# Optimization experiments

Measured on AMD Instinct MI355X. Metric: run time of the kernel, lower is better.

The kernel has to match this reference:

```python
import jax, jax.numpy as jnp
import numpy as np

B, N, K, H, L = 2, 1024, 48, 128, 3
SCALE = 30.0


def _gelu(x):
    # torch.nn.GELU default is the exact erf formulation
    return jax.nn.gelu(x, approximate=False)


def _ln(x, g, b, eps=1e-5):
    mu = jnp.mean(x, axis=-1, keepdims=True)
    var = jnp.mean((x - mu) ** 2, axis=-1, keepdims=True)
    return g * (x - mu) * jax.lax.rsqrt(var + eps) + b


def _gather_nodes(nodes, idx):
    # nodes: [B,N,H], idx: [B,N,K] -> [B,N,K,H]
    b, n, k = idx.shape
    flat = idx.reshape(b, n * k)
    g = jnp.take_along_axis(nodes, flat[:, :, None], axis=1)
    return g.reshape(b, n, k, nodes.shape[-1])


def setup_inputs() -> dict:
    key = jax.random.key(0)
    ks = jax.random.split(key, 16)

    def w(k, shape, fan_in):
        return jax.random.normal(k, shape, jnp.float32) / np.sqrt(fan_in).astype(np.float32)

    kp = jax.random.split(ks[5], 9)
    inp = {
        "h_V": jax.random.normal(ks[0], (B, N, H), jnp.float32),
        "h_E": jax.random.normal(ks[1], (B, N, K, H), jnp.float32),
        "E_idx": jax.random.randint(ks[2], (B, N, K), 0, N),
        "mask_V": jnp.ones((B, N), jnp.float32),
        "mask_attend": jnp.ones((B, N, K), jnp.float32),
        # message MLP (node update): W1 [3H->H], W2, W3
        "W1": w(kp[0], (L, 3 * H, H), 3 * H), "b1": jnp.zeros((L, H), jnp.float32),
        "W2": w(kp[1], (L, H, H), H), "b2": jnp.zeros((L, H), jnp.float32),
        "W3": w(kp[2], (L, H, H), H), "b3": jnp.zeros((L, H), jnp.float32),
        # message MLP (edge update): W11 [3H->H], W12, W13
        "W11": w(kp[3], (L, 3 * H, H), 3 * H), "b11": jnp.zeros((L, H), jnp.float32),
        "W12": w(kp[4], (L, H, H), H), "b12": jnp.zeros((L, H), jnp.float32),
        "W13": w(kp[5], (L, H, H), H), "b13": jnp.zeros((L, H), jnp.float32),
        # position-wise FFN: H -> 4H -> H
        "Win": w(kp[6], (L, H, 4 * H), H), "bin_": jnp.zeros((L, 4 * H), jnp.float32),
        "Wout": w(kp[7], (L, 4 * H, H), 4 * H), "bout": jnp.zeros((L, H), jnp.float32),
        # LayerNorms
        "g1": jnp.ones((L, H), jnp.float32), "be1": jnp.zeros((L, H), jnp.float32),
        "g2": jnp.ones((L, H), jnp.float32), "be2": jnp.zeros((L, H), jnp.float32),
        "g3": jnp.ones((L, H), jnp.float32), "be3": jnp.zeros((L, H), jnp.float32),
    }
    return inp


def reference(h_V, h_E, E_idx, mask_V, mask_attend,
              W1, b1, W2, b2, W3, b3,
              W11, b11, W12, b12, W13, b13,
              Win, bin_, Wout, bout,
              g1, be1, g2, be2, g3, be3):
    # Stack of L EncLayers (eval mode, dropout = identity).
    for l in range(L):
        # --- node update: gather neighbors, concat, 3-layer MLP message ---
        hVn = _gather_nodes(h_V, E_idx)                        # [B,N,K,H]
        hVe = jnp.broadcast_to(h_V[:, :, None, :], hVn.shape)  # [B,N,K,H]
        h_EV = jnp.concatenate([hVe, h_E, hVn], axis=-1)       # [B,N,K,3H]
        m = _gelu(h_EV @ W1[l] + b1[l])
        m = _gelu(m @ W2[l] + b2[l])
        m = m @ W3[l] + b3[l]
        m = mask_attend[..., None] * m
        dh = jnp.sum(m, axis=-2) / SCALE                       # masked sum aggregate
        h_V = _ln(h_V + dh, g1[l], be1[l])
        dh = _gelu(h_V @ Win[l] + bin_[l]) @ Wout[l] + bout[l]
        h_V = _ln(h_V + dh, g2[l], be2[l])
        h_V = mask_V[..., None] * h_V
        # --- edge update ---
        hVn = _gather_nodes(h_V, E_idx)
        hVe = jnp.broadcast_to(h_V[:, :, None, :], hVn.shape)
        h_EV = jnp.concatenate([hVe, h_E, hVn], axis=-1)
        m = _gelu(h_EV @ W11[l] + b11[l])
        m = _gelu(m @ W12[l] + b12[l])
        m = m @ W13[l] + b13[l]
        h_E = _ln(h_E + m, g3[l], be3[l])
    return h_V, h_E
```

## Files before the change

### kernel.cpp

```cpp
#include <hip/hip_runtime.h>
#include <hip/hip_bf16.h>
#include <math.h>

#define BB 2
#define NN 1024
#define HH 128
#define LL 3
#define SY 136
#define SH 520
#define SX 136
#define SM 132

typedef __attribute__((ext_vector_type(8))) short s8v;
typedef __attribute__((ext_vector_type(4))) float f4v;
typedef unsigned short u16;

static __device__ __forceinline__ u16 f2bf(float x) {
  union { float f; unsigned u; } v; v.f = x;
  unsigned r = v.u + 0x7FFFu + ((v.u >> 16) & 1u);
  return (u16)(r >> 16);
}
static __device__ __forceinline__ float geluf(float x) {
  float x2 = x * x;
  float u2 = x * (1.5957691216f + 0.0713548163f * x2);
  float e = __expf(u2);
  float d = __builtin_amdgcn_rcpf(e + 1.0f);
  return x - x * d;
}

static __device__ __forceinline__ void loadB(const u16* __restrict__ Wt, int wave, int lane,
                                             s8v B0[4], s8v B1[4]) {
  const int g = lane >> 4, q = lane & 15;
  const u16* wb0 = Wt + (wave * 32 + q) * 128 + g * 8;
  const u16* wb1 = wb0 + 16 * 128;
#pragma unroll
  for (int t = 0; t < 4; ++t) { B0[t] = *(const s8v*)(wb0 + t * 32); B1[t] = *(const s8v*)(wb1 + t * 32); }
}

static __device__ __forceinline__ void gemmA(const u16* __restrict__ A,
                                             const s8v B0[4], const s8v B1[4],
                                             int lane, f4v acc[3][2]) {
  const int g = lane >> 4, q = lane & 15;
  __builtin_amdgcn_s_setprio(1);
#pragma unroll
  for (int t = 0; t < 4; ++t) {
    const u16* Ab = A + t * 32 + g * 8;
    s8v a0 = *(const s8v*)(Ab + q * SY);
    s8v a1 = *(const s8v*)(Ab + (16 + q) * SY);
    s8v a2 = *(const s8v*)(Ab + (32 + q) * SY);
    acc[0][0] = __builtin_amdgcn_mfma_f32_16x16x32_bf16(a0, B0[t], acc[0][0], 0, 0, 0);
    acc[0][1] = __builtin_amdgcn_mfma_f32_16x16x32_bf16(a0, B1[t], acc[0][1], 0, 0, 0);
    acc[1][0] = __builtin_amdgcn_mfma_f32_16x16x32_bf16(a1, B0[t], acc[1][0], 0, 0, 0);
    acc[1][1] = __builtin_amdgcn_mfma_f32_16x16x32_bf16(a1, B1[t], acc[1][1], 0, 0, 0);
    acc[2][0] = __builtin_amdgcn_mfma_f32_16x16x32_bf16(a2, B0[t], acc[2][0], 0, 0, 0);
    acc[2][1] = __builtin_amdgcn_mfma_f32_16x16x32_bf16(a2, B1[t], acc[2][1], 0, 0, 0);
  }
  __builtin_amdgcn_s_setprio(0);
}

static __device__ __forceinline__ void gemm48k128(const u16* __restrict__ A,
                                                  const u16* __restrict__ Wt,
                                                  int wave, int lane, f4v acc[3][2]) {
  const int g = lane >> 4, q = lane & 15;
  s8v B0[4], B1[4];
  const u16* wb0 = Wt + (wave * 32 + q) * 128 + g * 8;
  const u16* wb1 = wb0 + 16 * 128;
#pragma unroll
  for (int t = 0; t < 4; ++t) { B0[t] = *(const s8v*)(wb0 + t * 32); B1[t] = *(const s8v*)(wb1 + t * 32); }
#pragma unroll
  for (int t = 0; t < 4; ++t) {
    const u16* Ab = A + t * 32 + g * 8;
    s8v a0 = *(const s8v*)(Ab + q * SY);
    s8v a1 = *(const s8v*)(Ab + (16 + q) * SY);
    s8v a2 = *(const s8v*)(Ab + (32 + q) * SY);
    acc[0][0] = __builtin_amdgcn_mfma_f32_16x16x32_bf16(a0, B0[t], acc[0][0], 0, 0, 0);
    acc[0][1] = __builtin_amdgcn_mfma_f32_16x16x32_bf16(a0, B1[t], acc[0][1], 0, 0, 0);
    acc[1][0] = __builtin_amdgcn_mfma_f32_16x16x32_bf16(a1, B0[t], acc[1][0], 0, 0, 0);
    acc[1][1] = __builtin_amdgcn_mfma_f32_16x16x32_bf16(a1, B1[t], acc[1][1], 0, 0, 0);
    acc[2][0] = __builtin_amdgcn_mfma_f32_16x16x32_bf16(a2, B0[t], acc[2][0], 0, 0, 0);
    acc[2][1] = __builtin_amdgcn_mfma_f32_16x16x32_bf16(a2, B1[t], acc[2][1], 0, 0, 0);
  }
}

static __device__ __forceinline__ void zero_acc(f4v acc[3][2]) {
#pragma unroll
  for (int rt = 0; rt < 3; ++rt)
#pragma unroll
    for (int c = 0; c < 2; ++c) acc[rt][c] = (f4v){0.f, 0.f, 0.f, 0.f};
}

static __device__ __forceinline__ void store_act(const f4v acc[3][2], u16* __restrict__ Y,
                                                 int wave, int lane, const float* __restrict__ bias) {
  const int g = lane >> 4, q = lane & 15;
#pragma unroll
  for (int c = 0; c < 2; ++c) {
    const int col = wave * 32 + c * 16 + q;
    const float bv = bias[col];
#pragma unroll
    for (int rt = 0; rt < 3; ++rt)
#pragma unroll
      for (int r = 0; r < 4; ++r) {
        const int row = rt * 16 + g * 4 + r;
        Y[row * SY + col] = f2bf(geluf(acc[rt][c][r] + bv));
      }
  }
}

static __device__ __forceinline__ void stage_f32(u16* __restrict__ dst, const float* src, int tid) {
  const float4* hEr = (const float4*)src;
#pragma unroll
  for (int p = 0; p < 6; ++p) {
    int i = tid + p * 256; int row = i >> 5, c = i & 31;
    float4 v = hEr[i];
    uint2 pk;
    pk.x = (unsigned)f2bf(v.x) | ((unsigned)f2bf(v.y) << 16);
    pk.y = (unsigned)f2bf(v.z) | ((unsigned)f2bf(v.w) << 16);
    *(uint2*)(dst + row * SY + c * 4) = pk;
  }
}

static __device__ __forceinline__ void init_acc(f4v acc[3][2],
                                                const float* __restrict__ Q, const float* __restrict__ P,
                                                const int* __restrict__ eidx, int bid, int bbase,
                                                int wave, int g, int q) {
  const float* Qr = Q + (size_t)bid * 128;
  const float qv0 = Qr[wave * 32 + q];
  const float qv1 = Qr[wave * 32 + 16 + q];
#pragma unroll
  for (int rt = 0; rt < 3; ++rt)
#pragma unroll
    for (int r = 0; r < 4; ++r) {
      const int row = rt * 16 + g * 4 + r;
      const int idx = eidx[bid * 48 + row];
      const float* Pr = P + (size_t)(bbase + idx) * 128 + wave * 32;
      acc[rt][0][r] = qv0 + Pr[q];
      acc[rt][1][r] = qv1 + Pr[16 + q];
    }
}

__global__ void conv_weights(const float* __restrict__ W1, const float* __restrict__ W2,
                             const float* __restrict__ W3, const float* __restrict__ W11,
                             const float* __restrict__ W12, const float* __restrict__ W13,
                             const float* __restrict__ Win, const float* __restrict__ Wout,
                             const float* __restrict__ hV,
                             u16* __restrict__ W1bT, u16* __restrict__ W2t,
                             u16* __restrict__ W3t, u16* __restrict__ W11bT,
                             u16* __restrict__ W12t, u16* __restrict__ W13t,
                             u16* __restrict__ Wint, u16* __restrict__ Woutt,
                             u16* __restrict__ PRE, u16* __restrict__ hv0bf) {
  const int tid = blockIdx.x * blockDim.x + threadIdx.x;
  const int nt = gridDim.x * blockDim.x;
  for (int i = tid; i < LL * 128 * 128; i += nt) {
    int l = i >> 14, rem = i & 16383;
    int k = rem >> 7, n = rem & 127;
    const int o = (l * 128 + n) * 128 + k;
    const int s = l * 16384 + k * 128 + n;
    W1bT [o] = f2bf(W1 [l * 49152 + (128 + k) * 128 + n]);
    W11bT[o] = f2bf(W11[l * 49152 + (128 + k) * 128 + n]);
    W2t [o] = f2bf(W2 [s]);
    W3t [o] = f2bf(W3 [s]);
    W12t[o] = f2bf(W12[s]);
    W13t[o] = f2bf(W13[s]);
    const int ln = (l + 1 == LL) ? 0 : l + 1;
    PRE[l * 65536 + (0 * 128 + n) * 128 + k] = f2bf(W11[l * 49152 + k * 128 + n]);
    PRE[l * 65536 + (1 * 128 + n) * 128 + k] = f2bf(W11[l * 49152 + (256 + k) * 128 + n]);
    PRE[l * 65536 + (2 * 128 + n) * 128 + k] = f2bf(W1 [ln * 49152 + k * 128 + n]);
    PRE[l * 65536 + (3 * 128 + n) * 128 + k] = f2bf(W1 [ln * 49152 + (256 + k) * 128 + n]);
  }
  for (int i = tid; i < LL * 128 * 512; i += nt) {
    int l = i / (128 * 512), rem = i - l * 128 * 512;
    int k = rem / 512, u = rem - k * 512;
    Wint[(l * 512 + u) * 128 + k] = f2bf(Win[i]);
  }
  for (int i = tid; i < LL * 512 * 128; i += nt) {
    int l = i / (512 * 128), rem = i - l * 512 * 128;
    int k = rem / 128, n = rem - k * 128;
    Woutt[(l * 128 + n) * 512 + k] = f2bf(Wout[i]);
  }
  for (int i = tid; i < BB * NN * HH; i += nt) hv0bf[i] = f2bf(hV[i]);
}

__global__ __launch_bounds__(256) void pre_kernel(const u16* __restrict__ hvbf,
                                                  const u16* __restrict__ Wq,
                                                  const u16* __restrict__ Wp,
                                                  float* __restrict__ Q, float* __restrict__ P) {
  __shared__ __align__(16) u16 shX[16 * SX];
  const int tid = threadIdx.x, lane = tid & 63, wave = tid >> 6;
  const int g = lane >> 4, q = lane & 15;
  const int r0 = blockIdx.x * 16;
  { int row = tid >> 4, c = tid & 15;
    *(uint4*)(shX + row * SX + c * 8) = ((const uint4*)(hvbf + (size_t)r0 * 128))[tid]; }
  __syncthreads();
  s8v af[4];
#pragma unroll
  for (int t = 0; t < 4; ++t) af[t] = *(const s8v*)(shX + q * SX + t * 32 + g * 8);
  const u16* W = (wave < 2) ? Wq : Wp;
  float* D = (wave < 2) ? Q : P;
  const int c0 = (wave & 1) * 64;
#pragma unroll
  for (int cf = 0; cf < 4; ++cf) {
    const int col = c0 + cf * 16 + q;
    const u16* wb = W + (size_t)col * 128 + g * 8;
    f4v acc = (f4v){0.f, 0.f, 0.f, 0.f};
#pragma unroll
    for (int t = 0; t < 4; ++t)
      acc = __builtin_amdgcn_mfma_f32_16x16x32_bf16(af[t], *(const s8v*)(wb + t * 32), acc, 0, 0, 0);
#pragma unroll
    for (int r = 0; r < 4; ++r) D[(size_t)(r0 + g * 4 + r) * 128 + col] = acc[r];
  }
}

__global__ __launch_bounds__(256, 6) void node_msg(
    const float* __restrict__ hv_res, const float* __restrict__ Qn, const float* __restrict__ Pn,
    const float* hE_src, const int* __restrict__ eidx, const float* __restrict__ mask_att,
    const u16* __restrict__ W1bT, const u16* __restrict__ W2t, const u16* __restrict__ W3t,
    const float* __restrict__ b1, const float* __restrict__ b2, const float* __restrict__ b3,
    const float* __restrict__ g1, const float* __restrict__ be1,
    float* __restrict__ hv1, u16* __restrict__ hv1bf) {
  __shared__ __align__(16) u16 buf[2 * 48 * SY];
  __shared__ float sh_mask[48];
  __shared__ float sh_x[128];
  __shared__ float sh_st[2];
  u16* bufA = buf;
  u16* bufB = buf + 48 * SY;

  const int tid = threadIdx.x, lane = tid & 63, wave = tid >> 6;
  const int g = lane >> 4, q = lane & 15;
  const int bid = blockIdx.x, bbase = bid & ~(NN - 1);

  if (tid < 48) sh_mask[tid] = mask_att[bid * 48 + tid];
  f4v acc[3][2];
  init_acc(acc, Qn, Pn, eidx, bid, bbase, wave, g, q);
  stage_f32(bufA, hE_src + (size_t)bid * 6144, tid);
  s8v Ba[4], Bb[4];
  loadB(W1bT, wave, lane, Ba, Bb);
  __syncthreads();

  gemmA(bufA, Ba, Bb, lane, acc);
  loadB(W2t, wave, lane, Ba, Bb);
  store_act(acc, bufB, wave, lane, b1);
  __syncthreads();

  zero_acc(acc);
  gemmA(bufB, Ba, Bb, lane, acc);
  loadB(W3t, wave, lane, Ba, Bb);
  store_act(acc, bufA, wave, lane, b2);
  __syncthreads();

  zero_acc(acc);
  gemmA(bufA, Ba, Bb, lane, acc);

  float msum = 0.f;
#pragma unroll
  for (int k = 0; k < 48; ++k) msum += sh_mask[k];
  float p0 = 0.f, p1 = 0.f;
#pragma unroll
  for (int rt = 0; rt < 3; ++rt)
#pragma unroll
    for (int r = 0; r < 4; ++r) {
      const float mk = sh_mask[rt * 16 + g * 4 + r];
      p0 += acc[rt][0][r] * mk;
      p1 += acc[rt][1][r] * mk;
    }
  p0 += __shfl_xor(p0, 16); p0 += __shfl_xor(p0, 32);
  p1 += __shfl_xor(p1, 16); p1 += __shfl_xor(p1, 32);
  if (g == 0) {
    const int c0 = wave * 32 + q, c1 = wave * 32 + 16 + q;
    sh_x[c0] = hv_res[(size_t)bid * 128 + c0] + (p0 + b3[c0] * msum) * (1.f / 30.f);
    sh_x[c1] = hv_res[(size_t)bid * 128 + c1] + (p1 + b3[c1] * msum) * (1.f / 30.f);
  }
  __syncthreads();

  if (tid < 64) {
    float a = sh_x[tid], c2 = sh_x[tid + 64];
    float s = a + c2, ss = a * a + c2 * c2;
#pragma unroll
    for (int off = 32; off; off >>= 1) { s += __shfl_xor(s, off); ss += __shfl_xor(ss, off); }
    if (tid == 0) { float mu = s * (1.f / 128.f); sh_st[0] = mu; sh_st[1] = ss * (1.f / 128.f) - mu * mu; }
  }
  __syncthreads();
  if (tid < 128) {
    float mu = sh_st[0], rs = rsqrtf(sh_st[1] + 1e-5f);
    float v = g1[tid] * (sh_x[tid] - mu) * rs + be1[tid];
    hv1[(size_t)bid * 128 + tid] = v;
    hv1bf[(size_t)bid * 128 + tid] = f2bf(v);
  }
}

__global__ __launch_bounds__(256) void ffn_kernel(
    const float* __restrict__ hv1, const u16* __restrict__ hv1bf,
    const u16* __restrict__ Wint, const float* __restrict__ binp,
    const u16* __restrict__ Woutt, const float* __restrict__ boutp,
    const float* __restrict__ g2, const float* __restrict__ be2,
    const float* __restrict__ mask_V,
    const u16* __restrict__ PRE,
    float* __restrict__ hv2,
    float* __restrict__ Qe, float* __restrict__ Pe,
    float* __restrict__ QnN, float* __restrict__ PnN) {
  __shared__ __align__(16) u16 shX[16 * SX];
  __shared__ __align__(16) u16 shH[16 * SH];
  __shared__ float shM[8 * 128];
  const int tid = threadIdx.x, lane = tid & 63, wave = tid >> 6;
  const int g = lane >> 4, q = lane & 15;
  const int r0 = blockIdx.x * 8;

  {
    int row = tid >> 4, c = tid & 15;
    uint4 v = (uint4){0, 0, 0, 0};
    if (tid < 128) v = ((const uint4*)(hv1bf + (size_t)r0 * 128))[tid];
    *(uint4*)(shX + row * SX + c * 8) = v;
  }
  __syncthreads();

  s8v a[4];
#pragma unroll
  for (int t = 0; t < 4; ++t) a[t] = *(const s8v*)(shX + q * SX + t * 32 + g * 8);
#pragma unroll
  for (int cf = 0; cf < 8; ++cf) {
    const int u = wave * 128 + cf * 16 + q;
    const u16* wb = Wint + (size_t)u * 128 + g * 8;
    f4v acc = (f4v){0.f, 0.f, 0.f, 0.f};
#pragma unroll
    for (int t = 0; t < 4; ++t)
      acc = __builtin_amdgcn_mfma_f32_16x16x32_bf16(a[t], *(const s8v*)(wb + t * 32), acc, 0, 0, 0);
    const float bv = binp[u];
#pragma unroll
    for (int r = 0; r < 4; ++r) shH[(g * 4 + r) * SH + u] = f2bf(geluf(acc[r] + bv));
  }
  __syncthreads();

#pragma unroll
  for (int c = 0; c < 2; ++c) {
    const int col = wave * 32 + c * 16 + q;
    const u16* wb = Woutt + (size_t)col * 512 + g * 8;
    s8v Bv[16];
#pragma unroll
    for (int t = 0; t < 16; ++t) Bv[t] = *(const s8v*)(wb + t * 32);
    f4v acc = (f4v){0.f, 0.f, 0.f, 0.f};
#pragma unroll
    for (int t = 0; t < 16; ++t) {
      s8v av = *(const s8v*)(shH + q * SH + t * 32 + g * 8);
      acc = __builtin_amdgcn_mfma_f32_16x16x32_bf16(av, Bv[t], acc, 0, 0, 0);
    }
    const float bv = boutp[col];
#pragma unroll
    for (int r = 0; r < 4; ++r) {
      const int row = g * 4 + r;
      if (row < 8) shM[row * 128 + col] = acc[r] + bv;
    }
  }
  __syncthreads();

#pragma unroll
  for (int i = 0; i < 2; ++i) {
    const int row = wave * 2 + i, gr = r0 + row;
    float x0 = hv1[(size_t)gr * 128 + lane]      + shM[row * 128 + lane];
    float x1 = hv1[(size_t)gr * 128 + 64 + lane] + shM[row * 128 + 64 + lane];
    float s = x0 + x1, ss = x0 * x0 + x1 * x1;
#pragma unroll
    for (int off = 32; off; off >>= 1) { s += __shfl_xor(s, off); ss += __shfl_xor(ss, off); }
    const float mu = s * (1.f / 128.f);
    const float rs = rsqrtf(ss * (1.f / 128.f) - mu * mu + 1e-5f);
    const float mv = mask_V[gr];
    float o0 = mv * (g2[lane]      * (x0 - mu) * rs + be2[lane]);
    float o1 = mv * (g2[lane + 64] * (x1 - mu) * rs + be2[lane + 64]);
    hv2[(size_t)gr * 128 + lane] = o0;
    hv2[(size_t)gr * 128 + 64 + lane] = o1;
    shX[row * SX + lane] = f2bf(o0);
    shX[row * SX + 64 + lane] = f2bf(o1);
  }
  __syncthreads();

  s8v af[4];
#pragma unroll
  for (int t = 0; t < 4; ++t) af[t] = *(const s8v*)(shX + q * SX + t * 32 + g * 8);
  float* dst = (wave == 0) ? Qe : (wave == 1) ? Pe : (wave == 2) ? QnN : PnN;
  const u16* Wb = PRE + (size_t)(wave * 128) * 128;
#pragma unroll
  for (int cf = 0; cf < 8; ++cf) {
    const int colr = cf * 16 + q;
    const u16* wb = Wb + (size_t)colr * 128 + g * 8;
    f4v acc = (f4v){0.f, 0.f, 0.f, 0.f};
#pragma unroll
    for (int t = 0; t < 4; ++t)
      acc = __builtin_amdgcn_mfma_f32_16x16x32_bf16(af[t], *(const s8v*)(wb + t * 32), acc, 0, 0, 0);
    if (g < 2) {
#pragma unroll
      for (int r = 0; r < 4; ++r)
        dst[(size_t)(r0 + g * 4 + r) * 128 + colr] = acc[r];
    }
  }
}

__global__ __launch_bounds__(256, 5) void edge_kernel(
    const float* __restrict__ Qe, const float* __restrict__ Pe,
    const float* hE_src, const int* __restrict__ eidx,
    const u16* __restrict__ W11bT, const u16* __restrict__ W12t, const u16* __restrict__ W13t,
    const float* __restrict__ b11, const float* __restrict__ b12, const float* __restrict__ b13,
    const float* __restrict__ g3, const float* __restrict__ be3,
    float* hE_out) {
  __shared__ __align__(16) u16 buf[2 * 48 * SY];
  __shared__ float2 sh_stats[48 * 4];
  __shared__ float2 sh_statsF[48];
  __shared__ int sh_idx[48];
  u16* bufA = buf;
  u16* bufB = buf + 48 * SY;

  const int tid = threadIdx.x, lane = tid & 63, wave = tid >> 6;
  const int g = lane >> 4, q = lane & 15;
  const int bid = blockIdx.x, bbase = bid & ~(NN - 1);

  if (tid < 48) sh_idx[tid] = eidx[bid * 48 + tid];
  stage_f32(bufA, hE_src + (size_t)bid * 6144, tid);
  __syncthreads();

  f4v acc[3][2];
  {
    const float* Qr = Qe + (size_t)bid * 128;
#pragma unroll
    for (int c = 0; c < 2; ++c) {
      const int col = wave * 32 + c * 16 + q;
      const float qv = Qr[col];
#pragma unroll
      for (int rt = 0; rt < 3; ++rt)
#pragma unroll
        for (int r = 0; r < 4; ++r) {
          const int row = rt * 16 + g * 4 + r;
          acc[rt][c][r] = qv + Pe[(size_t)(bbase + sh_idx[row]) * 128 + col];
        }
    }
  }
  gemm48k128(bufA, W11bT, wave, lane, acc);
  store_act(acc, bufB, wave, lane, b11);
  __syncthreads();

  zero_acc(acc);
  gemm48k128(bufB, W12t, wave, lane, acc);
  store_act(acc, bufA, wave, lane, b12);
  __syncthreads();

  const float* heb = hE_src + (size_t)bid * 6144;
  float xh[3][2][4];
#pragma unroll
  for (int rt = 0; rt < 3; ++rt)
#pragma unroll
    for (int c = 0; c < 2; ++c)
#pragma unroll
      for (int r = 0; r < 4; ++r)
        xh[rt][c][r] = heb[(rt * 16 + g * 4 + r) * 128 + wave * 32 + c * 16 + q];
  zero_acc(acc);
  gemm48k128(bufA, W13t, wave, lane, acc);
  const float bv0 = b13[wave * 32 + q], bv1 = b13[wave * 32 + 16 + q];
#pragma unroll
  for (int rt = 0; rt < 3; ++rt)
#pragma unroll
    for (int r = 0; r < 4; ++r) {
      xh[rt][0][r] += acc[rt][0][r] + bv0;
      xh[rt][1][r] += acc[rt][1][r] + bv1;
    }

#pragma unroll
  for (int rt = 0; rt < 3; ++rt)
#pragma unroll
    for (int r = 0; r < 4; ++r) {
      float s = xh[rt][0][r] + xh[rt][1][r];
      float ss = xh[rt][0][r] * xh[rt][0][r] + xh[rt][1][r] * xh[rt][1][r];
#pragma unroll
      for (int off = 1; off < 16; off <<= 1) { s += __shfl_xor(s, off); ss += __shfl_xor(ss, off); }
      if (q == 0) sh_stats[(rt * 16 + g * 4 + r) * 4 + wave] = make_float2(s, ss);
    }
  __syncthreads();
  if (tid < 48) {
    float s = 0.f, ss = 0.f;
#pragma unroll
    for (int w = 0; w < 4; ++w) { float2 v = sh_stats[tid * 4 + w]; s += v.x; ss += v.y; }
    float mu = s * (1.f / 128.f);
    float rs = rsqrtf(ss * (1.f / 128.f) - mu * mu + 1e-5f);
    sh_statsF[tid] = make_float2(mu, rs);
  }
  __syncthreads();

  float* shOut = (float*)buf;
  const float g30 = g3[wave * 32 + q], g31 = g3[wave * 32 + 16 + q];
  const float be30 = be3[wave * 32 + q], be31 = be3[wave * 32 + 16 + q];
#pragma unroll
  for (int rt = 0; rt < 3; ++rt)
#pragma unroll
    for (int r = 0; r < 4; ++r) {
      const int row = rt * 16 + g * 4 + r;
      const float2 mf = sh_statsF[row];
      shOut[row * SM + wave * 32 + q]      = g30 * (xh[rt][0][r] - mf.x) * mf.y + be30;
      shOut[row * SM + wave * 32 + 16 + q] = g31 * (xh[rt][1][r] - mf.x) * mf.y + be31;
    }
  __syncthreads();

  float4* wdst = (float4*)(hE_out + (size_t)bid * 6144);
#pragma unroll
  for (int p = 0; p < 6; ++p) {
    const int i = tid + p * 256;
    const int row = i >> 5, c4 = i & 31;
    wdst[i] = *(const float4*)(shOut + row * SM + 4 * c4);
  }
}

extern "C" void kernel_launch(void* const* d_in, const int* in_sizes, int n_in,
                              void* d_out, int out_size, void* d_ws, size_t ws_size,
                              hipStream_t stream) {
  const float* h_V      = (const float*)d_in[0];
  const float* h_E      = (const float*)d_in[1];
  const int*   E_idx    = (const int*)d_in[2];
  const float* mask_V   = (const float*)d_in[3];
  const float* mask_att = (const float*)d_in[4];
  const float* W1   = (const float*)d_in[5];   const float* b1   = (const float*)d_in[6];
  const float* W2   = (const float*)d_in[7];   const float* b2   = (const float*)d_in[8];
  const float* W3   = (const float*)d_in[9];   const float* b3   = (const float*)d_in[10];
  const float* W11  = (const float*)d_in[11];  const float* b11  = (const float*)d_in[12];
  const float* W12  = (const float*)d_in[13];  const float* b12  = (const float*)d_in[14];
  const float* W13  = (const float*)d_in[15];  const float* b13  = (const float*)d_in[16];
  const float* Win  = (const float*)d_in[17];  const float* binp = (const float*)d_in[18];
  const float* Wout = (const float*)d_in[19];  const float* boutp= (const float*)d_in[20];
  const float* g1   = (const float*)d_in[21];  const float* be1  = (const float*)d_in[22];
  const float* g2   = (const float*)d_in[23];  const float* be2  = (const float*)d_in[24];
  const float* g3   = (const float*)d_in[25];  const float* be3  = (const float*)d_in[26];

  float* outV = (float*)d_out;
  float* outE = outV + (size_t)BB * NN * HH;

  u16* ws     = (u16*)d_ws;
  u16* W1bT   = ws;
  u16* W11bT  = W1bT  + 3 * 16384;
  u16* W2t    = W11bT + 3 * 16384;
  u16* W3t    = W2t   + 3 * 16384;
  u16* W12t   = W3t   + 3 * 16384;
  u16* W13t   = W12t  + 3 * 16384;
  u16* Wint   = W13t  + 3 * 16384;
  u16* Woutt  = Wint  + 3 * 65536;
  u16* PREb   = Woutt + 3 * 65536;
  u16* hv0bf  = PREb  + 3 * 65536;
  u16* Pbf    = hv0bf + BB * NN * HH;
  float* Pf   = (float*)(Pbf + BB * NN * HH);
  float* Qf   = Pf  + BB * NN * HH;
  float* Qn   = Qf  + BB * NN * HH;
  float* Pn   = Qn  + BB * NN * HH;
  float* Qe   = Pn  + BB * NN * HH;
  float* Pe   = Qe  + BB * NN * HH;

  conv_weights<<<512, 256, 0, stream>>>(W1, W2, W3, W11, W12, W13, Win, Wout, h_V,
                                        W1bT, W2t, W3t, W11bT, W12t, W13t, Wint, Woutt,
                                        PREb, hv0bf);

  pre_kernel<<<(BB * NN) / 16, 256, 0, stream>>>(
      hv0bf, PREb + 2 * 65536 + 2 * 16384, PREb + 2 * 65536 + 3 * 16384, Qn, Pn);

  for (int l = 0; l < LL; ++l) {
    const float* hv_res  = (l == 0) ? h_V : Qf;
    const float* hE_src  = (l == 0) ? h_E : outE;
    float*       hv2_dst = (l == 2) ? outV : Qf;

    node_msg<<<BB * NN, 256, 0, stream>>>(
        hv_res, Qn, Pn, hE_src, E_idx, mask_att,
        W1bT + l * 16384, W2t + l * 16384, W3t + l * 16384,
        b1 + l * 128, b2 + l * 128, b3 + l * 128,
        g1 + l * 128, be1 + l * 128,
        Pf, Pbf);

    ffn_kernel<<<(BB * NN) / 8, 256, 0, stream>>>(
        Pf, Pbf,
        Wint + l * 65536, binp + l * 512,
        Woutt + l * 65536, boutp + l * 128,
        g2 + l * 128, be2 + l * 128, mask_V,
        PREb + l * 65536,
        hv2_dst, Qe, Pe, Qn, Pn);

    edge_kernel<<<BB * NN, 256, 0, stream>>>(
        Qe, Pe, hE_src, E_idx,
        W11bT + l * 16384, W12t + l * 16384, W13t + l * 16384,
        b11 + l * 128, b12 + l * 128, b13 + l * 128,
        g3 + l * 128, be3 + l * 128,
        outE);
  }
}
```

Baseline: 292.9 us.

## Split edge kernel into 16-row blocks across a 3-way grid dimension

Each edge-update block now handles 16 of the 48 neighbor rows of a node, and the grid triples in size via blockIdx.y. Per-block LDS and register use drop, and the launch bound rises to allow more resident blocks, aiming for more parallelism and better latency hiding. In exchange, every block reloads the full W11/W12/W13 weight fragments, so weight traffic triples and each MFMA B-operand load is amortised over fewer rows.

Measured after the change: 393.4 us. +34.3%, slower.

```diff
diff --git a/kernel.cpp b/kernel.cpp
--- a/kernel.cpp
+++ b/kernel.cpp
@@ -58,9 +58,9 @@
   __builtin_amdgcn_s_setprio(0);
 }
 
-static __device__ __forceinline__ void gemm48k128(const u16* __restrict__ A,
+static __device__ __forceinline__ void gemm16k128(const u16* __restrict__ A,
                                                   const u16* __restrict__ Wt,
-                                                  int wave, int lane, f4v acc[3][2]) {
+                                                  int wave, int lane, f4v acc[2]) {
   const int g = lane >> 4, q = lane & 15;
   s8v B0[4], B1[4];
   const u16* wb0 = Wt + (wave * 32 + q) * 128 + g * 8;
@@ -69,16 +69,9 @@
   for (int t = 0; t < 4; ++t) { B0[t] = *(const s8v*)(wb0 + t * 32); B1[t] = *(const s8v*)(wb1 + t * 32); }
 #pragma unroll
   for (int t = 0; t < 4; ++t) {
-    const u16* Ab = A + t * 32 + g * 8;
-    s8v a0 = *(const s8v*)(Ab + q * SY);
-    s8v a1 = *(const s8v*)(Ab + (16 + q) * SY);
-    s8v a2 = *(const s8v*)(Ab + (32 + q) * SY);
-    acc[0][0] = __builtin_amdgcn_mfma_f32_16x16x32_bf16(a0, B0[t], acc[0][0], 0, 0, 0);
-    acc[0][1] = __builtin_amdgcn_mfma_f32_16x16x32_bf16(a0, B1[t], acc[0][1], 0, 0, 0);
-    acc[1][0] = __builtin_amdgcn_mfma_f32_16x16x32_bf16(a1, B0[t], acc[1][0], 0, 0, 0);
-    acc[1][1] = __builtin_amdgcn_mfma_f32_16x16x32_bf16(a1, B1[t], acc[1][1], 0, 0, 0);
-    acc[2][0] = __builtin_amdgcn_mfma_f32_16x16x32_bf16(a2, B0[t], acc[2][0], 0, 0, 0);
-    acc[2][1] = __builtin_amdgcn_mfma_f32_16x16x32_bf16(a2, B1[t], acc[2][1], 0, 0, 0);
+    s8v a0 = *(const s8v*)(A + q * SY + t * 32 + g * 8);
+    acc[0] = __builtin_amdgcn_mfma_f32_16x16x32_bf16(a0, B0[t], acc[0], 0, 0, 0);
+    acc[1] = __builtin_amdgcn_mfma_f32_16x16x32_bf16(a0, B1[t], acc[1], 0, 0, 0);
   }
 }
 
@@ -103,6 +96,19 @@
         const int row = rt * 16 + g * 4 + r;
         Y[row * SY + col] = f2bf(geluf(acc[rt][c][r] + bv));
       }
+  }
+}
+
+static __device__ __forceinline__ void store_act16(const f4v acc[2], u16* __restrict__ Y,
+                                                   int wave, int lane, const float* __restrict__ bias) {
+  const int g = lane >> 4, q = lane & 15;
+#pragma unroll
+  for (int c = 0; c < 2; ++c) {
+    const int col = wave * 32 + c * 16 + q;
+    const float bv = bias[col];
+#pragma unroll
+    for (int r = 0; r < 4; ++r)
+      Y[(g * 4 + r) * SY + col] = f2bf(geluf(acc[c][r] + bv));
   }
 }
 
@@ -392,85 +398,86 @@
   }
 }
 
-__global__ __launch_bounds__(256, 5) void edge_kernel(
+__global__ __launch_bounds__(256, 6) void edge_kernel(
     const float* __restrict__ Qe, const float* __restrict__ Pe,
     const float* hE_src, const int* __restrict__ eidx,
     const u16* __restrict__ W11bT, const u16* __restrict__ W12t, const u16* __restrict__ W13t,
     const float* __restrict__ b11, const float* __restrict__ b12, const float* __restrict__ b13,
     const float* __restrict__ g3, const float* __restrict__ be3,
     float* hE_out) {
-  __shared__ __align__(16) u16 buf[2 * 48 * SY];
-  __shared__ float2 sh_stats[48 * 4];
-  __shared__ float2 sh_statsF[48];
-  __shared__ int sh_idx[48];
+  __shared__ __align__(16) u16 buf[2 * 16 * SY];
+  __shared__ float2 sh_stats[16 * 4];
+  __shared__ float2 sh_statsF[16];
   u16* bufA = buf;
-  u16* bufB = buf + 48 * SY;
+  u16* bufB = buf + 16 * SY;
 
   const int tid = threadIdx.x, lane = tid & 63, wave = tid >> 6;
   const int g = lane >> 4, q = lane & 15;
-  const int bid = blockIdx.x, bbase = bid & ~(NN - 1);
-
-  if (tid < 48) sh_idx[tid] = eidx[bid * 48 + tid];
-  stage_f32(bufA, hE_src + (size_t)bid * 6144, tid);
-  __syncthreads();
-
-  f4v acc[3][2];
+  const int node = blockIdx.x, row0 = blockIdx.y * 16;
+  const int bbase = node & ~(NN - 1);
+
+  f4v acc[2];
   {
-    const float* Qr = Qe + (size_t)bid * 128;
-#pragma unroll
-    for (int c = 0; c < 2; ++c) {
-      const int col = wave * 32 + c * 16 + q;
-      const float qv = Qr[col];
-#pragma unroll
-      for (int rt = 0; rt < 3; ++rt)
-#pragma unroll
-        for (int r = 0; r < 4; ++r) {
-          const int row = rt * 16 + g * 4 + r;
-          acc[rt][c][r] = qv + Pe[(size_t)(bbase + sh_idx[row]) * 128 + col];
-        }
-    }
-  }
-  gemm48k128(bufA, W11bT, wave, lane, acc);
-  store_act(acc, bufB, wave, lane, b11);
-  __syncthreads();
-
-  zero_acc(acc);
-  gemm48k128(bufB, W12t, wave, lane, acc);
-  store_act(acc, bufA, wave, lane, b12);
-  __syncthreads();
-
-  const float* heb = hE_src + (size_t)bid * 6144;
-  float xh[3][2][4];
-#pragma unroll
-  for (int rt = 0; rt < 3; ++rt)
-#pragma unroll
-    for (int c = 0; c < 2; ++c)
-#pragma unroll
-      for (int r = 0; r < 4; ++r)
-        xh[rt][c][r] = heb[(rt * 16 + g * 4 + r) * 128 + wave * 32 + c * 16 + q];
-  zero_acc(acc);
-  gemm48k128(bufA, W13t, wave, lane, acc);
+    const float* Qr = Qe + (size_t)node * 128;
+    const float qv0 = Qr[wave * 32 + q];
+    const float qv1 = Qr[wave * 32 + 16 + q];
+#pragma unroll
+    for (int r = 0; r < 4; ++r) {
+      const int idx = eidx[node * 48 + row0 + g * 4 + r];
+      const float* Pr = Pe + (size_t)(bbase + idx) * 128 + wave * 32;
+      acc[0][r] = qv0 + Pr[q];
+      acc[1][r] = qv1 + Pr[16 + q];
+    }
+  }
+  {
+    const float4* hEr = (const float4*)(hE_src + (size_t)node * 6144) + row0 * 32;
+#pragma unroll
+    for (int p = 0; p < 2; ++p) {
+      int i = tid + p * 256; int row = i >> 5, c = i & 31;
+      float4 v = hEr[i];
+      uint2 pk;
+      pk.x = (unsigned)f2bf(v.x) | ((unsigned)f2bf(v.y) << 16);
+      pk.y = (unsigned)f2bf(v.z) | ((unsigned)f2bf(v.w) << 16);
+      *(uint2*)(bufA + row * SY + c * 4) = pk;
+    }
+  }
+  __syncthreads();
+
+  gemm16k128(bufA, W11bT, wave, lane, acc);
+  store_act16(acc, bufB, wave, lane, b11);
+  __syncthreads();
+
+  acc[0] = (f4v){0.f, 0.f, 0.f, 0.f}; acc[1] = (f4v){0.f, 0.f, 0.f, 0.f};
+  gemm16k128(bufB, W12t, wave, lane, acc);
+  store_act16(acc, bufA, wave, lane, b12);
+  __syncthreads();
+
+  const float* heb = hE_src + (size_t)node * 6144 + (size_t)row0 * 128;
+  float xh[2][4];
+#pragma unroll
+  for (int c = 0; c < 2; ++c)
+#pragma unroll
+    for (int r = 0; r < 4; ++r)
+      xh[c][r] = heb[(g * 4 + r) * 128 + wave * 32 + c * 16 + q];
+  acc[0] = (f4v){0.f, 0.f, 0.f, 0.f}; acc[1] = (f4v){0.f, 0.f, 0.f, 0.f};
+  gemm16k128(bufA, W13t, wave, lane, acc);
   const float bv0 = b13[wave * 32 + q], bv1 = b13[wave * 32 + 16 + q];
 #pragma unroll
-  for (int rt = 0; rt < 3; ++rt)
-#pragma unroll
-    for (int r = 0; r < 4; ++r) {
-      xh[rt][0][r] += acc[rt][0][r] + bv0;
-      xh[rt][1][r] += acc[rt][1][r] + bv1;
-    }
-
-#pragma unroll
-  for (int rt = 0; rt < 3; ++rt)
-#pragma unroll
-    for (int r = 0; r < 4; ++r) {
-      float s = xh[rt][0][r] + xh[rt][1][r];
-      float ss = xh[rt][0][r] * xh[rt][0][r] + xh[rt][1][r] * xh[rt][1][r];
-#pragma unroll
-      for (int off = 1; off < 16; off <<= 1) { s += __shfl_xor(s, off); ss += __shfl_xor(ss, off); }
-      if (q == 0) sh_stats[(rt * 16 + g * 4 + r) * 4 + wave] = make_float2(s, ss);
-    }
-  __syncthreads();
-  if (tid < 48) {
+  for (int r = 0; r < 4; ++r) {
+    xh[0][r] += acc[0][r] + bv0;
+    xh[1][r] += acc[1][r] + bv1;
+  }
+
+#pragma unroll
+  for (int r = 0; r < 4; ++r) {
+    float s = xh[0][r] + xh[1][r];
+    float ss = xh[0][r] * xh[0][r] + xh[1][r] * xh[1][r];
+#pragma unroll
+    for (int off = 1; off < 16; off <<= 1) { s += __shfl_xor(s, off); ss += __shfl_xor(ss, off); }
+    if (q == 0) sh_stats[(g * 4 + r) * 4 + wave] = make_float2(s, ss);
+  }
+  __syncthreads();
+  if (tid < 16) {
     float s = 0.f, ss = 0.f;
 #pragma unroll
     for (int w = 0; w < 4; ++w) { float2 v = sh_stats[tid * 4 + w]; s += v.x; ss += v.y; }
@@ -484,19 +491,17 @@
   const float g30 = g3[wave * 32 + q], g31 = g3[wave * 32 + 16 + q];
   const float be30 = be3[wave * 32 + q], be31 = be3[wave * 32 + 16 + q];
 #pragma unroll
-  for (int rt = 0; rt < 3; ++rt)
-#pragma unroll
-    for (int r = 0; r < 4; ++r) {
-      const int row = rt * 16 + g * 4 + r;
-      const float2 mf = sh_statsF[row];
-      shOut[row * SM + wave * 32 + q]      = g30 * (xh[rt][0][r] - mf.x) * mf.y + be30;
-      shOut[row * SM + wave * 32 + 16 + q] = g31 * (xh[rt][1][r] - mf.x) * mf.y + be31;
-    }
-  __syncthreads();
-
-  float4* wdst = (float4*)(hE_out + (size_t)bid * 6144);
-#pragma unroll
-  for (int p = 0; p < 6; ++p) {
+  for (int r = 0; r < 4; ++r) {
+    const int row = g * 4 + r;
+    const float2 mf = sh_statsF[row];
+    shOut[row * SM + wave * 32 + q]      = g30 * (xh[0][r] - mf.x) * mf.y + be30;
+    shOut[row * SM + wave * 32 + 16 + q] = g31 * (xh[1][r] - mf.x) * mf.y + be31;
+  }
+  __syncthreads();
+
+  float4* wdst = (float4*)(hE_out + (size_t)node * 6144) + row0 * 32;
+#pragma unroll
+  for (int p = 0; p < 2; ++p) {
     const int i = tid + p * 256;
     const int row = i >> 5, c4 = i & 31;
     wdst[i] = *(const float4*)(shOut + row * SM + 4 * c4);
@@ -572,7 +577,7 @@
         PREb + l * 65536,
         hv2_dst, Qe, Pe, Qn, Pn);
 
-    edge_kernel<<<BB * NN, 256, 0, stream>>>(
+    edge_kernel<<<dim3(BB * NN, 3), 256, 0, stream>>>(
         Qe, Pe, hE_src, E_idx,
         W11bT + l * 16384, W12t + l * 16384, W13t + l * 16384,
         b11 + l * 128, b12 + l * 128, b13 + l * 128,
```

## Prefetch next weight fragments during edge GEMMs and shrink edge kernel LDS

Applied to the files above, without the earlier changes.

The edge kernel now loads each layer's weight fragments into registers (loadB) before the preceding store/barrier, so global weight loads overlap MFMA work and the epilogue instead of stalling at the start of each GEMM. Accumulator initialization no longer goes through a shared index table, which removes a barrier. The stats scratch now aliases bufB, and the occupancy hint rises from 5 to 6 blocks. Register pressure rises from holding prefetched fragments, which could cause spills under the tighter launch bound.

Measured after the change: 311.9 us. 6.5% more time.

```diff
diff --git a/kernel.cpp b/kernel.cpp
--- a/kernel.cpp
+++ b/kernel.cpp
@@ -56,30 +56,6 @@
     acc[2][1] = __builtin_amdgcn_mfma_f32_16x16x32_bf16(a2, B1[t], acc[2][1], 0, 0, 0);
   }
   __builtin_amdgcn_s_setprio(0);
-}
-
-static __device__ __forceinline__ void gemm48k128(const u16* __restrict__ A,
-                                                  const u16* __restrict__ Wt,
-                                                  int wave, int lane, f4v acc[3][2]) {
-  const int g = lane >> 4, q = lane & 15;
-  s8v B0[4], B1[4];
-  const u16* wb0 = Wt + (wave * 32 + q) * 128 + g * 8;
-  const u16* wb1 = wb0 + 16 * 128;
-#pragma unroll
-  for (int t = 0; t < 4; ++t) { B0[t] = *(const s8v*)(wb0 + t * 32); B1[t] = *(const s8v*)(wb1 + t * 32); }
-#pragma unroll
-  for (int t = 0; t < 4; ++t) {
-    const u16* Ab = A + t * 32 + g * 8;
-    s8v a0 = *(const s8v*)(Ab + q * SY);
-    s8v a1 = *(const s8v*)(Ab + (16 + q) * SY);
-    s8v a2 = *(const s8v*)(Ab + (32 + q) * SY);
-    acc[0][0] = __builtin_amdgcn_mfma_f32_16x16x32_bf16(a0, B0[t], acc[0][0], 0, 0, 0);
-    acc[0][1] = __builtin_amdgcn_mfma_f32_16x16x32_bf16(a0, B1[t], acc[0][1], 0, 0, 0);
-    acc[1][0] = __builtin_amdgcn_mfma_f32_16x16x32_bf16(a1, B0[t], acc[1][0], 0, 0, 0);
-    acc[1][1] = __builtin_amdgcn_mfma_f32_16x16x32_bf16(a1, B1[t], acc[1][1], 0, 0, 0);
-    acc[2][0] = __builtin_amdgcn_mfma_f32_16x16x32_bf16(a2, B0[t], acc[2][0], 0, 0, 0);
-    acc[2][1] = __builtin_amdgcn_mfma_f32_16x16x32_bf16(a2, B1[t], acc[2][1], 0, 0, 0);
-  }
 }
 
 static __device__ __forceinline__ void zero_acc(f4v acc[3][2]) {
@@ -392,7 +368,7 @@
   }
 }
 
-__global__ __launch_bounds__(256, 5) void edge_kernel(
+__global__ __launch_bounds__(256, 6) void edge_kernel(
     const float* __restrict__ Qe, const float* __restrict__ Pe,
     const float* hE_src, const int* __restrict__ eidx,
     const u16* __restrict__ W11bT, const u16* __restrict__ W12t, const u16* __restrict__ W13t,
@@ -400,42 +376,30 @@
     const float* __restrict__ g3, const float* __restrict__ be3,
     float* hE_out) {
   __shared__ __align__(16) u16 buf[2 * 48 * SY];
-  __shared__ float2 sh_stats[48 * 4];
   __shared__ float2 sh_statsF[48];
-  __shared__ int sh_idx[48];
   u16* bufA = buf;
   u16* bufB = buf + 48 * SY;
+  float2* sh_stats = (float2*)bufB;
 
   const int tid = threadIdx.x, lane = tid & 63, wave = tid >> 6;
   const int g = lane >> 4, q = lane & 15;
   const int bid = blockIdx.x, bbase = bid & ~(NN - 1);
 
-  if (tid < 48) sh_idx[tid] = eidx[bid * 48 + tid];
+  f4v acc[3][2];
+  init_acc(acc, Qe, Pe, eidx, bid, bbase, wave, g, q);
   stage_f32(bufA, hE_src + (size_t)bid * 6144, tid);
-  __syncthreads();
-
-  f4v acc[3][2];
-  {
-    const float* Qr = Qe + (size_t)bid * 128;
-#pragma unroll
-    for (int c = 0; c < 2; ++c) {
-      const int col = wave * 32 + c * 16 + q;
-      const float qv = Qr[col];
-#pragma unroll
-      for (int rt = 0; rt < 3; ++rt)
-#pragma unroll
-        for (int r = 0; r < 4; ++r) {
-          const int row = rt * 16 + g * 4 + r;
-          acc[rt][c][r] = qv + Pe[(size_t)(bbase + sh_idx[row]) * 128 + col];
-        }
-    }
-  }
-  gemm48k128(bufA, W11bT, wave, lane, acc);
+  s8v Ba[4], Bb[4];
+  loadB(W11bT, wave, lane, Ba, Bb);
+  __syncthreads();
+
+  gemmA(bufA, Ba, Bb, lane, acc);
+  loadB(W12t, wave, lane, Ba, Bb);
   store_act(acc, bufB, wave, lane, b11);
   __syncthreads();
 
   zero_acc(acc);
-  gemm48k128(bufB, W12t, wave, lane, acc);
+  gemmA(bufB, Ba, Bb, lane, acc);
+  loadB(W13t, wave, lane, Ba, Bb);
   store_act(acc, bufA, wave, lane, b12);
   __syncthreads();
 
@@ -449,7 +413,7 @@
       for (int r = 0; r < 4; ++r)
         xh[rt][c][r] = heb[(rt * 16 + g * 4 + r) * 128 + wave * 32 + c * 16 + q];
   zero_acc(acc);
-  gemm48k128(bufA, W13t, wave, lane, acc);
+  gemmA(bufA, Ba, Bb, lane, acc);
   const float bv0 = b13[wave * 32 + q], bv1 = b13[wave * 32 + 16 + q];
 #pragma unroll
   for (int rt = 0; rt < 3; ++rt)
```
